# Performance work log

Measured on AMD Instinct MI355X. Metric: run time of the kernel, lower is better.

The kernel has to match this reference:

```python
import jax, jax.numpy as jnp
import numpy as np

B, NN, NC, CARD = 2048, 24, 8, 16
D, H, L, FH, K, DOUT = 512, 8, 3, 1024, 64, 1
S = NN + NC + 1  # M features + CLS token (appended last)
DH = D // H


def _ln(x, w, b):
    m = x.mean(-1, keepdims=True)
    v = ((x - m) ** 2).mean(-1, keepdims=True)
    return (x - m) / jnp.sqrt(v + 1e-5) * w + b


def _build_masks():
    # k random feature-feature interaction pairs per block (seed = attention_seed + block),
    # plus the diagonal and full CLS row/column (CLS is the last token).
    masks = np.zeros((L, S, S), dtype=bool)
    for l in range(L):
        rng = np.random.default_rng(42 + l)
        m = np.zeros((S, S), dtype=bool)
        np.fill_diagonal(m, True)
        m[S - 1, :] = True
        m[:, S - 1] = True
        M = S - 1
        for _ in range(K):
            i, j = rng.integers(0, M, size=2)
            m[i, j] = True
            m[j, i] = True
        masks[l] = m
    return jnp.asarray(masks)


def setup_inputs() -> dict:
    key = jax.random.key(0)
    cnt = [0]

    def nrm(shape, scale=0.02):
        cnt[0] += 1
        return jax.random.normal(jax.random.fold_in(key, cnt[0]), shape, jnp.float32) * scale

    inp = {}
    inp["x_num"] = jax.random.normal(jax.random.fold_in(key, 1000), (B, NN), jnp.float32)
    inp["x_cat"] = jax.random.randint(jax.random.fold_in(key, 1001), (B, NC), 0, CARD)
    # FeatureTokenizer params
    inp["w_num"] = nrm((NN, D), 0.1)
    inp["b_num"] = nrm((NN, D), 0.1)
    inp["emb_cat"] = nrm((NC * CARD, D), 0.1)
    inp["b_cat"] = nrm((NC, D), 0.1)
    inp["cls"] = nrm((D,), 0.1)
    # block params stacked over L blocks
    inp["ln1_w"] = jnp.ones((L, D)); inp["ln1_b"] = jnp.zeros((L, D))
    inp["Wq"] = nrm((L, D, D)); inp["bq"] = jnp.zeros((L, D))
    inp["Wk"] = nrm((L, D, D)); inp["bk"] = jnp.zeros((L, D))
    inp["Wv"] = nrm((L, D, D)); inp["bv"] = jnp.zeros((L, D))
    inp["Wo"] = nrm((L, D, D)); inp["bo"] = jnp.zeros((L, D))
    inp["ln2_w"] = jnp.ones((L, D)); inp["ln2_b"] = jnp.zeros((L, D))
    inp["Wf1"] = nrm((L, D, 2 * FH)); inp["bf1"] = jnp.zeros((L, 2 * FH))
    inp["Wf2"] = nrm((L, FH, D)); inp["bf2"] = jnp.zeros((L, D))
    inp["mask"] = _build_masks()
    inp["cat_offsets"] = jnp.arange(NC) * CARD
    # head params
    inp["hln_w"] = jnp.ones((D,)); inp["hln_b"] = jnp.zeros((D,))
    inp["Wh"] = nrm((D, DOUT)); inp["bh"] = jnp.zeros((DOUT,))
    return inp


def reference(x_num, x_cat, w_num, b_num, emb_cat, b_cat, cls, ln1_w, ln1_b, Wq, bq, Wk, bk, Wv, bv, Wo, bo, ln2_w, ln2_b, Wf1, bf1, Wf2, bf2, mask, cat_offsets, hln_w, hln_b, Wh, bh):
    b = x_num.shape[0]
    tok_num = x_num[:, :, None] * w_num[None] + b_num[None]          # [B, NN, D]
    tok_cat = emb_cat[x_cat + cat_offsets[None]] + b_cat[None]       # [B, NC, D]
    x = jnp.concatenate([tok_num, tok_cat, jnp.broadcast_to(cls, (b, 1, D))], axis=1)  # [B, S, D]
    scale = 1.0 / jnp.sqrt(jnp.asarray(DH, x.dtype))
    for l in range(L):
        # sparse random attention (prenorm)
        h = _ln(x, ln1_w[l], ln1_b[l])
        q = (h @ Wq[l] + bq[l]).reshape(b, S, H, DH)
        k = (h @ Wk[l] + bk[l]).reshape(b, S, H, DH)
        v = (h @ Wv[l] + bv[l]).reshape(b, S, H, DH)
        scores = jnp.einsum('bihd,bjhd->bhij', q, k) * scale
        scores = jnp.where(mask[l][None, None], scores, jnp.asarray(-1e9, scores.dtype))
        attn = jax.nn.softmax(scores, axis=-1)
        o = jnp.einsum('bhij,bjhd->bihd', attn, v).reshape(b, S, D)
        x = x + (o @ Wo[l] + bo[l])
        # ReGLU FFN (prenorm)
        h = _ln(x, ln2_w[l], ln2_b[l])
        f = h @ Wf1[l] + bf1[l]
        a, g = jnp.split(f, 2, axis=-1)
        x = x + ((a * jax.nn.relu(g)) @ Wf2[l] + bf2[l])
    # head on CLS token (last position): LayerNorm -> ReLU -> Linear
    c = _ln(x[:, -1], hln_w, hln_b)
    return jax.nn.relu(c) @ Wh + bh
```

## Files before the change

### kernel.cpp

```cpp
#include <hip/hip_runtime.h>
#include <stdint.h>

#define Bq    2048
#define NNq   24
#define NCq   8
#define CARDq 16
#define Dq    512
#define Hq    8
#define Lq    3
#define FHq   1024
#define Sq    33

typedef unsigned short u16;
typedef unsigned int   u32;
typedef __bf16 bf16x8 __attribute__((ext_vector_type(8)));
typedef float  f32x4  __attribute__((ext_vector_type(4)));

__device__ __forceinline__ u16 f2bf(float f) {
  u32 u = __builtin_bit_cast(u32, f);
  u = (u + 0x7fffu + ((u >> 16) & 1u)) >> 16;
  return (u16)u;
}
__device__ __forceinline__ float bf2f(u16 h) {
  u32 u = ((u32)h) << 16;
  return __builtin_bit_cast(float, u);
}

__device__ __forceinline__ void glds16(const void* g, void* l) {
  __builtin_amdgcn_global_load_lds((const __attribute__((address_space(1))) void*)g,
                                   (__attribute__((address_space(3))) void*)l, 16, 0, 0);
}

__global__ __launch_bounds__(256) void wconv_all_kernel(const float* __restrict__ Wq,
                                                        const float* __restrict__ Wk,
                                                        const float* __restrict__ Wv,
                                                        const float* __restrict__ Wo,
                                                        const float* __restrict__ Wf1,
                                                        const float* __restrict__ Wf2,
                                                        u16* __restrict__ WqkvT,
                                                        u16* __restrict__ WoT,
                                                        u16* __restrict__ Wf1T,
                                                        u16* __restrict__ Wf2T) {
  __shared__ float tile[32][33];
  const int l = blockIdx.y;
  int id = blockIdx.x;
  const float* src; u16* dst; int K, N;
  if (id < 768) {
    const int m = id >> 8; id &= 255;
    src = ((m == 0) ? Wq : (m == 1) ? Wk : Wv) + (size_t)l * 262144;
    dst = WqkvT + (size_t)l * 786432 + (size_t)m * 262144;
    K = 512; N = 512;
  } else if (id < 1024) {
    id -= 768;
    src = Wo + (size_t)l * 262144;  dst = WoT + (size_t)l * 262144;
    K = 512; N = 512;
  } else if (id < 2048) {
    id -= 1024;
    src = Wf1 + (size_t)l * 1048576; dst = Wf1T + (size_t)l * 1048576;
    K = 512; N = 2048;
  } else {
    id -= 2048;
    src = Wf2 + (size_t)l * 524288;  dst = Wf2T + (size_t)l * 524288;
    K = 1024; N = 512;
  }
  const int ntn = N >> 5;
  const int n0 = (id % ntn) * 32, k0 = (id / ntn) * 32;
  const int tx = threadIdx.x & 31, ty = threadIdx.x >> 5;
#pragma unroll
  for (int r = 0; r < 32; r += 8)
    tile[ty + r][tx] = src[(size_t)(k0 + ty + r) * N + (n0 + tx)];
  __syncthreads();
#pragma unroll
  for (int r = 0; r < 32; r += 8)
    dst[(size_t)(n0 + ty + r) * K + (k0 + tx)] = f2bf(tile[tx][ty + r]);
}

__global__ __launch_bounds__(256) void tok_ln_kernel(const float* __restrict__ x_num,
                                                     const int* __restrict__ x_cat,
                                                     const float* __restrict__ w_num,
                                                     const float* __restrict__ b_num,
                                                     const float* __restrict__ emb_cat,
                                                     const float* __restrict__ b_cat,
                                                     const float* __restrict__ cls,
                                                     const float* __restrict__ gw,
                                                     const float* __restrict__ gb,
                                                     float* __restrict__ X,
                                                     u16* __restrict__ Hout, int c0) {
  const int wave = threadIdx.x >> 6, lane = threadIdx.x & 63;
  const int tok = blockIdx.x * 4 + wave;
  const int b   = tok / Sq;
  const int s   = tok - b * Sq;
  const int bg  = c0 + b;
  const int col0 = lane * 8;
  float v[8];
  if (s < NNq) {
    const float xv = x_num[bg * NNq + s];
    const float4 w0 = *(const float4*)(w_num + s * Dq + col0);
    const float4 w1 = *(const float4*)(w_num + s * Dq + col0 + 4);
    const float4 b0 = *(const float4*)(b_num + s * Dq + col0);
    const float4 b1 = *(const float4*)(b_num + s * Dq + col0 + 4);
    v[0]=fmaf(xv,w0.x,b0.x); v[1]=fmaf(xv,w0.y,b0.y); v[2]=fmaf(xv,w0.z,b0.z); v[3]=fmaf(xv,w0.w,b0.w);
    v[4]=fmaf(xv,w1.x,b1.x); v[5]=fmaf(xv,w1.y,b1.y); v[6]=fmaf(xv,w1.z,b1.z); v[7]=fmaf(xv,w1.w,b1.w);
  } else if (s < NNq + NCq) {
    const int j = s - NNq;
    const int row = x_cat[bg * NCq + j] + j * CARDq;
    const float4 e0 = *(const float4*)(emb_cat + (size_t)row * Dq + col0);
    const float4 e1 = *(const float4*)(emb_cat + (size_t)row * Dq + col0 + 4);
    const float4 b0 = *(const float4*)(b_cat + j * Dq + col0);
    const float4 b1 = *(const float4*)(b_cat + j * Dq + col0 + 4);
    v[0]=e0.x+b0.x; v[1]=e0.y+b0.y; v[2]=e0.z+b0.z; v[3]=e0.w+b0.w;
    v[4]=e1.x+b1.x; v[5]=e1.y+b1.y; v[6]=e1.z+b1.z; v[7]=e1.w+b1.w;
  } else {
    const float4 c0v = *(const float4*)(cls + col0);
    const float4 c1v = *(const float4*)(cls + col0 + 4);
    v[0]=c0v.x; v[1]=c0v.y; v[2]=c0v.z; v[3]=c0v.w;
    v[4]=c1v.x; v[5]=c1v.y; v[6]=c1v.z; v[7]=c1v.w;
  }
  float s1 = 0.f, s2 = 0.f;
#pragma unroll
  for (int i = 0; i < 8; i++) { s1 += v[i]; s2 += v[i] * v[i]; }
#pragma unroll
  for (int off = 32; off > 0; off >>= 1) { s1 += __shfl_xor(s1, off); s2 += __shfl_xor(s2, off); }
  const float mean = s1 * (1.0f / Dq);
  const float rstd = rsqrtf(s2 * (1.0f / Dq) - mean * mean + 1e-5f);
  float* xp = X + (size_t)tok * Dq + col0;
  *(float4*)xp       = (float4){v[0], v[1], v[2], v[3]};
  *(float4*)(xp + 4) = (float4){v[4], v[5], v[6], v[7]};
  const float* gwp = gw + col0;
  const float* gbp = gb + col0;
  u16 o[8];
#pragma unroll
  for (int i = 0; i < 8; i++) o[i] = f2bf((v[i] - mean) * rstd * gwp[i] + gbp[i]);
  uint4 pk;
  pk.x = (u32)o[0] | ((u32)o[1] << 16); pk.y = (u32)o[2] | ((u32)o[3] << 16);
  pk.z = (u32)o[4] | ((u32)o[5] << 16); pk.w = (u32)o[6] | ((u32)o[7] << 16);
  *(uint4*)(Hout + (size_t)tok * Dq + col0) = pk;
}

__global__ __launch_bounds__(256) void ln_kernel(const float* __restrict__ X,
                                                 const float* __restrict__ gw,
                                                 const float* __restrict__ gb,
                                                 u16* __restrict__ Hout,
                                                 int inmul, int inadd) {
  const int wave = threadIdx.x >> 6, lane = threadIdx.x & 63;
  const int row = blockIdx.x * 4 + wave;
  const size_t srow = (size_t)row * inmul + inadd;
  const float* xr = X + srow * Dq + lane * 8;
  const float4 a = *(const float4*)xr;
  const float4 b = *(const float4*)(xr + 4);
  float s  = a.x + a.y + a.z + a.w + b.x + b.y + b.z + b.w;
  float ss = a.x*a.x + a.y*a.y + a.z*a.z + a.w*a.w + b.x*b.x + b.y*b.y + b.z*b.z + b.w*b.w;
#pragma unroll
  for (int off = 32; off > 0; off >>= 1) { s += __shfl_xor(s, off); ss += __shfl_xor(ss, off); }
  const float mean = s * (1.0f / Dq);
  const float rstd = rsqrtf(ss * (1.0f / Dq) - mean * mean + 1e-5f);
  const float xv[8] = {a.x, a.y, a.z, a.w, b.x, b.y, b.z, b.w};
  const float* gwp = gw + lane * 8;
  const float* gbp = gb + lane * 8;
  u16 o[8];
#pragma unroll
  for (int i = 0; i < 8; i++) o[i] = f2bf((xv[i] - mean) * rstd * gwp[i] + gbp[i]);
  uint4 pk;
  pk.x = (u32)o[0] | ((u32)o[1] << 16); pk.y = (u32)o[2] | ((u32)o[3] << 16);
  pk.z = (u32)o[4] | ((u32)o[5] << 16); pk.w = (u32)o[6] | ((u32)o[7] << 16);
  *(uint4*)(Hout + (size_t)row * Dq + lane * 8) = pk;
}

template <int MODE>
__global__ __launch_bounds__(256) void gemm_kernel(const u16* __restrict__ A,
                                                   const u16* __restrict__ Bt0, const u16* __restrict__ Bt1, const u16* __restrict__ Bt2,
                                                   const float* __restrict__ bi0, const float* __restrict__ bi1, const float* __restrict__ bi2,
                                                   void* __restrict__ out0, void* __restrict__ out1, void* __restrict__ out2,
                                                   size_t ostride, int K, int amul, int aadd, int xmul, int xadd) {
  __shared__ uint4 smem4[1024];
  char* smem = (char*)smem4;
  const int tid  = threadIdx.x;
  const int wave = tid >> 6;
  const int lane = tid & 63;
  const int mblk = blockIdx.x;
  const int nblk = blockIdx.y;
  const u16*   Bt;
  const float* bias;
  void*        outp;
  if (MODE == 3) {
    Bt = Bt0; bias = nullptr; outp = out0;
  } else {
    const int z = blockIdx.z;
    Bt   = (z == 0) ? Bt0 : (z == 1) ? Bt1 : Bt2;
    bias = (z == 0) ? bi0 : (z == 1) ? bi1 : bi2;
    outp = (z == 0) ? out0 : (z == 1) ? out1 : out2;
  }

  const int cg   = (lane & 3) ^ ((lane >> 3) & 3);
  const int arow = wave * 32 + (lane >> 2);
  const u16* gA0 = A + ((size_t)(mblk * 128 + arow) * amul + aadd) * K + cg * 8;
  const u16* gA1 = A + ((size_t)(mblk * 128 + arow + 16) * amul + aadd) * K + cg * 8;
  char* lA0 = smem + wave * 2048;
  char* lA1 = lA0 + 1024;

  const u16 *gB0, *gB1;
  char *lB0, *lB1;
  if (MODE == 2) {
    const int brow = wave * 16 + (lane >> 2);
    gB0 = Bt + (size_t)(nblk * 64 + brow) * K + cg * 8;
    gB1 = Bt + (size_t)(FHq + nblk * 64 + brow) * K + cg * 8;
    lB0 = smem + 8192  + wave * 1024;
    lB1 = smem + 12288 + wave * 1024;
  } else {
    const int brow = wave * 32 + (lane >> 2);
    gB0 = Bt + (size_t)(nblk * 128 + brow) * K + cg * 8;
    gB1 = gB0 + (size_t)16 * K;
    lB0 = smem + 8192 + wave * 2048;
    lB1 = lB0 + 1024;
  }

  const int slot = (lane >> 4) ^ ((lane >> 1) & 3);
  const int r16  = lane & 15;
  const int wm   = (wave >> 1) * 64;
  int aoff[4], boff[4];
#pragma unroll
  for (int i = 0; i < 4; i++) aoff[i] = (wm + i * 16 + r16) * 64 + slot * 16;
  if (MODE == 2) {
    const int wn = (wave & 1) * 32;
#pragma unroll
    for (int j = 0; j < 2; j++) {
      boff[j]     = 8192  + (wn + j * 16 + r16) * 64 + slot * 16;
      boff[2 + j] = 12288 + (wn + j * 16 + r16) * 64 + slot * 16;
    }
  } else {
    const int wn = (wave & 1) * 64;
#pragma unroll
    for (int j = 0; j < 4; j++) boff[j] = 8192 + (wn + j * 16 + r16) * 64 + slot * 16;
  }

  f32x4 acc[16];
#pragma unroll
  for (int i = 0; i < 16; i++) acc[i] = (f32x4){0.f, 0.f, 0.f, 0.f};

  const int kiter = K >> 5;
  for (int kk = 0; kk < kiter; kk++) {
    __syncthreads();
    glds16(gA0, lA0); glds16(gA1, lA1);
    glds16(gB0, lB0); glds16(gB1, lB1);
    gA0 += 32; gA1 += 32; gB0 += 32; gB1 += 32;
    __syncthreads();

    if (MODE == 2) {
      bf16x8 af[4], ba[2], bg[2];
#pragma unroll
      for (int i = 0; i < 4; i++) af[i] = *(const bf16x8*)(smem + aoff[i]);
#pragma unroll
      for (int j = 0; j < 2; j++) {
        ba[j] = *(const bf16x8*)(smem + boff[j]);
        bg[j] = *(const bf16x8*)(smem + boff[2 + j]);
      }
#pragma unroll
      for (int i = 0; i < 4; i++)
#pragma unroll
        for (int j = 0; j < 2; j++) {
          acc[i * 2 + j]     = __builtin_amdgcn_mfma_f32_16x16x32_bf16(af[i], ba[j], acc[i * 2 + j], 0, 0, 0);
          acc[8 + i * 2 + j] = __builtin_amdgcn_mfma_f32_16x16x32_bf16(af[i], bg[j], acc[8 + i * 2 + j], 0, 0, 0);
        }
    } else {
      bf16x8 af[4], bf[4];
#pragma unroll
      for (int i = 0; i < 4; i++) af[i] = *(const bf16x8*)(smem + aoff[i]);
#pragma unroll
      for (int j = 0; j < 4; j++) bf[j] = *(const bf16x8*)(smem + boff[j]);
#pragma unroll
      for (int i = 0; i < 4; i++)
#pragma unroll
        for (int j = 0; j < 4; j++)
          acc[i * 4 + j] = __builtin_amdgcn_mfma_f32_16x16x32_bf16(af[i], bf[j], acc[i * 4 + j], 0, 0, 0);
    }
  }

  const int quad = lane >> 4;
  if (MODE == 3) {
    const int buf = nblk >> 2;
    u16* C = (u16*)out0 + (size_t)buf * ostride;
    const float* biasp = (buf == 0) ? bi0 : (buf == 1) ? bi1 : bi2;
    const int colbase = (nblk & 3) * 128 + (wave & 1) * 64;
#pragma unroll
    for (int j = 0; j < 4; j++) {
      const int c = colbase + j * 16 + r16;
      const float bv = biasp[c];
#pragma unroll
      for (int i = 0; i < 4; i++) {
        const int r0 = mblk * 128 + wm + i * 16 + quad * 4;
        f32x4 v = acc[i * 4 + j];
#pragma unroll
        for (int r = 0; r < 4; r++)
          C[(size_t)(r0 + r) * Dq + c] = f2bf(v[r] + bv);
      }
    }
  } else if (MODE == 1) {
    float* X = (float*)outp;
    const int wn = (wave & 1) * 64;
#pragma unroll
    for (int j = 0; j < 4; j++) {
      const int c = nblk * 128 + wn + j * 16 + r16;
      const float bv = bias[c];
#pragma unroll
      for (int i = 0; i < 4; i++) {
        const int r0 = mblk * 128 + wm + i * 16 + quad * 4;
        f32x4 v = acc[i * 4 + j];
#pragma unroll
        for (int r = 0; r < 4; r++) {
          const size_t idx = ((size_t)(r0 + r) * xmul + xadd) * Dq + c;
          X[idx] += v[r] + bv;
        }
      }
    }
  } else if (MODE == 2) {
    u16* AG = (u16*)outp;
    const int wn = (wave & 1) * 32;
#pragma unroll
    for (int j = 0; j < 2; j++) {
      const int c = nblk * 64 + wn + j * 16 + r16;
      const float bva = bias[c];
      const float bvg = bias[FHq + c];
#pragma unroll
      for (int i = 0; i < 4; i++) {
        const int r0 = mblk * 128 + wm + i * 16 + quad * 4;
        f32x4 va = acc[i * 2 + j];
        f32x4 vg = acc[8 + i * 2 + j];
#pragma unroll
        for (int r = 0; r < 4; r++) {
          const float av = va[r] + bva;
          const float gv = vg[r] + bvg;
          AG[(size_t)(r0 + r) * FHq + c] = f2bf(av * fmaxf(gv, 0.f));
        }
      }
    }
  }
}

__global__ __launch_bounds__(256) void attn_mfma_kernel(const u16* __restrict__ Q,
                                                        const u16* __restrict__ K,
                                                        const u16* __restrict__ V,
                                                        const void* __restrict__ maskp,
                                                        int l, u16* __restrict__ O) {
  __shared__ u16 lds_all[4][8064];
  const int wave = threadIdx.x >> 6, lane = threadIdx.x & 63;
  const int b = blockIdx.x >> 1;
  const int h = (blockIdx.x & 1) * 4 + wave;
  u16* VT = &lds_all[wave][0];
  u16* P  = &lds_all[wave][64 * 72];
  const size_t hbase = (size_t)b * (Sq * Dq) + (size_t)h * 64;
  const int r16 = lane & 15, quad = lane >> 4;

  const unsigned char* mu = (const unsigned char*)maskp + (size_t)l * (Sq * Sq);
  const int* mi = (const int*)maskp + (size_t)l * (Sq * Sq);
  int myok = 1;
  if (lane < Sq) myok = (mu[lane * (Sq + 1)] != 0) ? 1 : 0;
  const unsigned long long bal = __ballot(myok);
  const unsigned long long MM = (1ULL << Sq) - 1ULL;
  const int use_u8 = ((bal & MM) == MM) ? 1 : 0;

  const uint4 z4 = {0u, 0u, 0u, 0u};
  for (int t = lane; t < 576; t += 64) ((uint4*)VT)[t] = z4;
  for (int t = lane; t < 432; t += 64) ((uint4*)P)[t]  = z4;
  for (int t = lane; t < 264; t += 64) {
    const int j = t >> 3, ck = t & 7;
    const uint4 src = *(const uint4*)(V + hbase + (size_t)j * Dq + ck * 8);
    const u16* sp = (const u16*)&src;
#pragma unroll
    for (int e = 0; e < 8; e++) VT[(ck * 8 + e) * 72 + j] = sp[e];
  }
  __syncthreads();

  bf16x8 qf[3][2], kf[3][2];
#pragma unroll
  for (int m = 0; m < 3; m++) {
    const int rl = (m * 16 + r16 < Sq) ? (m * 16 + r16) : (Sq - 1);
#pragma unroll
    for (int kk = 0; kk < 2; kk++) {
      qf[m][kk] = *(const bf16x8*)(Q + hbase + (size_t)rl * Dq + kk * 32 + quad * 8);
      kf[m][kk] = *(const bf16x8*)(K + hbase + (size_t)rl * Dq + kk * 32 + quad * 8);
    }
  }
  f32x4 acc[3][3];
#pragma unroll
  for (int m = 0; m < 3; m++)
#pragma unroll
    for (int n = 0; n < 3; n++) acc[m][n] = (f32x4){0.f, 0.f, 0.f, 0.f};
#pragma unroll
  for (int kk = 0; kk < 2; kk++)
#pragma unroll
    for (int m = 0; m < 3; m++)
#pragma unroll
      for (int n = 0; n < 3; n++)
        acc[m][n] = __builtin_amdgcn_mfma_f32_16x16x32_bf16(qf[m][kk], kf[n][kk], acc[m][n], 0, 0, 0);

  float linv[3][4];
#pragma unroll
  for (int m = 0; m < 3; m++) {
    float v[3][4];
#pragma unroll
    for (int n = 0; n < 3; n++) {
      const int c = n * 16 + r16;
#pragma unroll
      for (int r = 0; r < 4; r++) {
        const int R = m * 16 + quad * 4 + r;
        float madd = -1e9f;
        if (R < Sq && c < Sq) {
          const int mv = use_u8 ? (int)mu[R * Sq + c] : mi[R * Sq + c];
          madd = mv ? 0.f : -1e9f;
        }
        v[n][r] = acc[m][n][r] * 0.125f + madd;
      }
    }
    float mr[4], sum[4];
#pragma unroll
    for (int r = 0; r < 4; r++) {
      mr[r] = fmaxf(fmaxf(v[0][r], v[1][r]), v[2][r]);
#pragma unroll
      for (int off = 8; off > 0; off >>= 1) mr[r] = fmaxf(mr[r], __shfl_xor(mr[r], off));
      sum[r] = 0.f;
    }
#pragma unroll
    for (int n = 0; n < 3; n++)
#pragma unroll
      for (int r = 0; r < 4; r++) { v[n][r] = __expf(v[n][r] - mr[r]); sum[r] += v[n][r]; }
#pragma unroll
    for (int r = 0; r < 4; r++) {
#pragma unroll
      for (int off = 8; off > 0; off >>= 1) sum[r] += __shfl_xor(sum[r], off);
      linv[m][r] = 1.0f / sum[r];
    }
#pragma unroll
    for (int n = 0; n < 3; n++)
#pragma unroll
      for (int r = 0; r < 4; r++)
        P[(m * 16 + quad * 4 + r) * 72 + n * 16 + r16] = f2bf(v[n][r]);
  }
  __syncthreads();

  bf16x8 pa[3][2], vb[4][2];
#pragma unroll
  for (int m = 0; m < 3; m++)
#pragma unroll
    for (int kk = 0; kk < 2; kk++)
      pa[m][kk] = *(const bf16x8*)(P + (m * 16 + r16) * 72 + kk * 32 + quad * 8);
#pragma unroll
  for (int n = 0; n < 4; n++)
#pragma unroll
    for (int kk = 0; kk < 2; kk++)
      vb[n][kk] = *(const bf16x8*)(VT + (n * 16 + r16) * 72 + kk * 32 + quad * 8);
  f32x4 o[3][4];
#pragma unroll
  for (int m = 0; m < 3; m++)
#pragma unroll
    for (int n = 0; n < 4; n++) o[m][n] = (f32x4){0.f, 0.f, 0.f, 0.f};
#pragma unroll
  for (int kk = 0; kk < 2; kk++)
#pragma unroll
    for (int m = 0; m < 3; m++)
#pragma unroll
      for (int n = 0; n < 4; n++)
        o[m][n] = __builtin_amdgcn_mfma_f32_16x16x32_bf16(pa[m][kk], vb[n][kk], o[m][n], 0, 0, 0);

#pragma unroll
  for (int m = 0; m < 3; m++)
#pragma unroll
    for (int r = 0; r < 4; r++) {
      const int i = m * 16 + quad * 4 + r;
      if (i < Sq) {
#pragma unroll
        for (int n = 0; n < 4; n++)
          O[hbase + (size_t)i * Dq + n * 16 + r16] = f2bf(o[m][n][r] * linv[m][r]);
      }
    }
}

__global__ __launch_bounds__(256) void head_kernel(const float* __restrict__ X,
                                                   const float* __restrict__ hw, const float* __restrict__ hb,
                                                   const float* __restrict__ Wh, const float* __restrict__ bh,
                                                   float* __restrict__ out) {
  const int wave = threadIdx.x >> 6, lane = threadIdx.x & 63;
  const int b = blockIdx.x * 4 + wave;
  const float* xr = X + ((size_t)b * Sq + (Sq - 1)) * Dq + lane * 8;
  const float4 a  = *(const float4*)xr;
  const float4 bb = *(const float4*)(xr + 4);
  const float xv[8] = {a.x, a.y, a.z, a.w, bb.x, bb.y, bb.z, bb.w};
  float s = 0.f, ss = 0.f;
#pragma unroll
  for (int i = 0; i < 8; i++) { s += xv[i]; ss += xv[i] * xv[i]; }
#pragma unroll
  for (int off = 32; off > 0; off >>= 1) { s += __shfl_xor(s, off); ss += __shfl_xor(ss, off); }
  const float mean = s * (1.0f / Dq);
  const float rstd = rsqrtf(ss * (1.0f / Dq) - mean * mean + 1e-5f);
  float part = 0.f;
#pragma unroll
  for (int i = 0; i < 8; i++) {
    const float c = (xv[i] - mean) * rstd * hw[lane * 8 + i] + hb[lane * 8 + i];
    part += fmaxf(c, 0.f) * Wh[lane * 8 + i];
  }
#pragma unroll
  for (int off = 32; off > 0; off >>= 1) part += __shfl_xor(part, off);
  if (lane == 0) out[b] = part + bh[0];
}

extern "C" void kernel_launch(void* const* d_in, const int* in_sizes, int n_in,
                              void* d_out, int out_size, void* d_ws, size_t ws_size,
                              hipStream_t stream) {
  (void)in_sizes; (void)n_in; (void)out_size;
  const float* x_num   = (const float*)d_in[0];
  const int*   x_cat   = (const int*)d_in[1];
  const float* w_num   = (const float*)d_in[2];
  const float* b_num   = (const float*)d_in[3];
  const float* emb_cat = (const float*)d_in[4];
  const float* b_cat   = (const float*)d_in[5];
  const float* cls     = (const float*)d_in[6];
  const float* ln1_w   = (const float*)d_in[7];
  const float* ln1_b   = (const float*)d_in[8];
  const float* Wq      = (const float*)d_in[9];
  const float* bq      = (const float*)d_in[10];
  const float* Wk      = (const float*)d_in[11];
  const float* bk      = (const float*)d_in[12];
  const float* Wv      = (const float*)d_in[13];
  const float* bv      = (const float*)d_in[14];
  const float* Wo      = (const float*)d_in[15];
  const float* bo      = (const float*)d_in[16];
  const float* ln2_w   = (const float*)d_in[17];
  const float* ln2_b   = (const float*)d_in[18];
  const float* Wf1     = (const float*)d_in[19];
  const float* bf1     = (const float*)d_in[20];
  const float* Wf2     = (const float*)d_in[21];
  const float* bf2     = (const float*)d_in[22];
  const void*  mask    = d_in[23];
  const float* hln_w   = (const float*)d_in[25];
  const float* hln_b   = (const float*)d_in[26];
  const float* Wh      = (const float*)d_in[27];
  const float* bhp     = (const float*)d_in[28];
  float* out = (float*)d_out;

  const size_t WBYTES = 15728640ULL;
  int Bc = Bq;
  while (Bc > 128) {
    const size_t need = WBYTES + (size_t)Bc * Sq * 6144ULL;
    if (need <= ws_size) break;
    Bc >>= 1;
  }
  const size_t Mc = (size_t)Bc * Sq;

  char* ws = (char*)d_ws;
  u16* Wbase = (u16*)ws;
  float* X   = (float*)(ws + WBYTES);
  u16* Hb    = (u16*)((char*)X + Mc * 2048);
  u16* Qb    = (u16*)((char*)Hb + Mc * 1024);
  u16* Kb    = Qb + Mc * 512;
  u16* Vb    = Kb + Mc * 512;
  u16* AGb   = Qb;

  u16* WqkvT = Wbase;
  u16* WoT   = WqkvT + 2359296;
  u16* Wf1T  = WoT   + 786432;
  u16* Wf2T  = Wf1T  + 3145728;

  wconv_all_kernel<<<dim3(2560, 3), 256, 0, stream>>>(Wq, Wk, Wv, Wo, Wf1, Wf2,
                                                      WqkvT, WoT, Wf1T, Wf2T);

  const int mb  = (int)(Mc / 128);
  const int mbC = Bc / 128;

  for (int c0 = 0; c0 < Bq; c0 += Bc) {
    tok_ln_kernel<<<(int)(Mc / 4), 256, 0, stream>>>(x_num, x_cat, w_num, b_num, emb_cat, b_cat, cls,
                                                     ln1_w, ln1_b, X, Hb, c0);

    for (int l = 0; l < Lq; l++) {
      gemm_kernel<3><<<dim3(mb, 12, 1), 256, 0, stream>>>(Hb,
          WqkvT + l * 786432, nullptr, nullptr,
          bq + l * 512, bk + l * 512, bv + l * 512,
          Qb, nullptr, nullptr, Mc * 512, 512, 1, 0, 1, 0);
      attn_mfma_kernel<<<Bc * 2, 256, 0, stream>>>(Qb, Kb, Vb, mask, l, Hb);

      if (l < Lq - 1) {
        gemm_kernel<1><<<dim3(mb, 4, 1), 256, 0, stream>>>(Hb,
            WoT + l * 262144, WoT + l * 262144, WoT + l * 262144,
            bo + l * 512, bo + l * 512, bo + l * 512,
            X, X, X, 0, 512, 1, 0, 1, 0);
        ln_kernel<<<(int)(Mc / 4), 256, 0, stream>>>(X, ln2_w + l * 512, ln2_b + l * 512, Hb, 1, 0);
        gemm_kernel<2><<<dim3(mb, 16, 1), 256, 0, stream>>>(Hb,
            Wf1T + l * 1048576, Wf1T + l * 1048576, Wf1T + l * 1048576,
            bf1 + l * 2048, bf1 + l * 2048, bf1 + l * 2048,
            AGb, AGb, AGb, 0, 512, 1, 0, 1, 0);
        gemm_kernel<1><<<dim3(mb, 4, 1), 256, 0, stream>>>(AGb,
            Wf2T + l * 524288, Wf2T + l * 524288, Wf2T + l * 524288,
            bf2 + l * 512, bf2 + l * 512, bf2 + l * 512,
            X, X, X, 0, 1024, 1, 0, 1, 0);
        ln_kernel<<<(int)(Mc / 4), 256, 0, stream>>>(X, ln1_w + (l + 1) * 512, ln1_b + (l + 1) * 512, Hb, 1, 0);
      } else {
        gemm_kernel<1><<<dim3(mbC, 4, 1), 256, 0, stream>>>(Hb,
            WoT + l * 262144, WoT + l * 262144, WoT + l * 262144,
            bo + l * 512, bo + l * 512, bo + l * 512,
            X, X, X, 0, 512, Sq, Sq - 1, Sq, Sq - 1);
        ln_kernel<<<Bc / 4, 256, 0, stream>>>(X, ln2_w + l * 512, ln2_b + l * 512, Kb, Sq, Sq - 1);
        gemm_kernel<2><<<dim3(mbC, 16, 1), 256, 0, stream>>>(Kb,
            Wf1T + l * 1048576, Wf1T + l * 1048576, Wf1T + l * 1048576,
            bf1 + l * 2048, bf1 + l * 2048, bf1 + l * 2048,
            AGb, AGb, AGb, 0, 512, 1, 0, 1, 0);
        gemm_kernel<1><<<dim3(mbC, 4, 1), 256, 0, stream>>>(AGb,
            Wf2T + l * 524288, Wf2T + l * 524288, Wf2T + l * 524288,
            bf2 + l * 512, bf2 + l * 512, bf2 + l * 512,
            X, X, X, 0, 1024, 1, 0, Sq, Sq - 1);
      }
    }
    head_kernel<<<Bc / 4, 256, 0, stream>>>(X, hln_w, hln_b, Wh, bhp, out + c0);
  }
}
```

Baseline: 2.186 ms.

## Compute only CLS query and CLS attention in last layer; swap GEMM grid axes

In the final block only the CLS token feeds the head, so Q projection and attention are computed just for the CLS row. K/V still come from all tokens via a column-offset GEMM, and a new per-head attention kernel computes the CLS row. The mask is dropped there because the CLS row attends to every token. GEMM grids also put the N-block on blockIdx.x so consecutive blocks share A tiles, which may help L2 reuse.

```diff
diff --git a/kernel.cpp b/kernel.cpp
--- a/kernel.cpp
+++ b/kernel.cpp
@@ -171,14 +171,14 @@
                                                    const u16* __restrict__ Bt0, const u16* __restrict__ Bt1, const u16* __restrict__ Bt2,
                                                    const float* __restrict__ bi0, const float* __restrict__ bi1, const float* __restrict__ bi2,
                                                    void* __restrict__ out0, void* __restrict__ out1, void* __restrict__ out2,
-                                                   size_t ostride, int K, int amul, int aadd, int xmul, int xadd) {
+                                                   size_t ostride, int K, int amul, int aadd, int xmul, int xadd, int nofs) {
   __shared__ uint4 smem4[1024];
   char* smem = (char*)smem4;
   const int tid  = threadIdx.x;
   const int wave = tid >> 6;
   const int lane = tid & 63;
-  const int mblk = blockIdx.x;
-  const int nblk = blockIdx.y;
+  const int mblk = blockIdx.y;
+  const int nblk = blockIdx.x;
   const u16*   Bt;
   const float* bias;
   void*        outp;
@@ -208,7 +208,7 @@
     lB1 = smem + 12288 + wave * 1024;
   } else {
     const int brow = wave * 32 + (lane >> 2);
-    gB0 = Bt + (size_t)(nblk * 128 + brow) * K + cg * 8;
+    gB0 = Bt + (size_t)((nblk + nofs) * 128 + brow) * K + cg * 8;
     gB1 = gB0 + (size_t)16 * K;
     lB0 = smem + 8192 + wave * 2048;
     lB1 = lB0 + 1024;
@@ -277,10 +277,11 @@
 
   const int quad = lane >> 4;
   if (MODE == 3) {
-    const int buf = nblk >> 2;
+    const int nb   = nblk + nofs;
+    const int buf  = nb >> 2;
     u16* C = (u16*)out0 + (size_t)buf * ostride;
     const float* biasp = (buf == 0) ? bi0 : (buf == 1) ? bi1 : bi2;
-    const int colbase = (nblk & 3) * 128 + (wave & 1) * 64;
+    const int colbase = (nb & 3) * 128 + (wave & 1) * 64;
 #pragma unroll
     for (int j = 0; j < 4; j++) {
       const int c = colbase + j * 16 + r16;
@@ -472,6 +473,57 @@
           O[hbase + (size_t)i * Dq + n * 16 + r16] = f2bf(o[m][n][r] * linv[m][r]);
       }
     }
+}
+
+__global__ __launch_bounds__(256) void attn_cls_kernel(const u16* __restrict__ Qc,
+                                                       const u16* __restrict__ Kf,
+                                                       const u16* __restrict__ Vf,
+                                                       u16* __restrict__ Oc) {
+  __shared__ u16 lds[4][4432];
+  __shared__ float psh[4][40];
+  const int wave = threadIdx.x >> 6, lane = threadIdx.x & 63;
+  const int b = blockIdx.x >> 1;
+  const int h = (blockIdx.x & 1) * 4 + wave;
+  u16* Kl = &lds[wave][0];
+  u16* Vl = &lds[wave][2178];
+  u16* ql = &lds[wave][4360];
+  const size_t hbase = (size_t)b * (Sq * Dq) + (size_t)h * 64;
+
+  for (int t = lane; t < 528; t += 64) {
+    const int mtx = (t >= 264) ? 1 : 0;
+    const int e = t - mtx * 264;
+    const int j = e >> 3, ck = e & 7;
+    const uint4 v = *(const uint4*)((mtx ? Vf : Kf) + hbase + (size_t)j * Dq + ck * 8);
+    u16* dst = (mtx ? Vl : Kl) + j * 66 + ck * 8;
+    const u16* sp = (const u16*)&v;
+#pragma unroll
+    for (int e2 = 0; e2 < 8; e2++) dst[e2] = sp[e2];
+  }
+  if (lane < 8)
+    *(uint4*)(ql + lane * 8) = *(const uint4*)(Qc + (size_t)b * Dq + h * 64 + lane * 8);
+  __syncthreads();
+
+  float p;
+  if (lane < Sq) {
+    float s = 0.f;
+#pragma unroll 16
+    for (int d = 0; d < 64; d++) s += bf2f(ql[d]) * bf2f(Kl[lane * 66 + d]);
+    p = s * 0.125f;
+  } else p = -3e38f;
+  float mx = p;
+#pragma unroll
+  for (int off = 32; off > 0; off >>= 1) mx = fmaxf(mx, __shfl_xor(mx, off));
+  float e = (lane < Sq) ? __expf(p - mx) : 0.f;
+  float sum = e;
+#pragma unroll
+  for (int off = 32; off > 0; off >>= 1) sum += __shfl_xor(sum, off);
+  if (lane < Sq) psh[wave][lane] = e / sum;
+  __syncthreads();
+
+  float o = 0.f;
+#pragma unroll
+  for (int j = 0; j < Sq; j++) o += psh[wave][j] * bf2f(Vl[j * 66 + lane]);
+  Oc[(size_t)b * Dq + h * 64 + lane] = f2bf(o);
 }
 
 __global__ __launch_bounds__(256) void head_kernel(const float* __restrict__ X,
@@ -570,41 +622,49 @@
                                                      ln1_w, ln1_b, X, Hb, c0);
 
     for (int l = 0; l < Lq; l++) {
-      gemm_kernel<3><<<dim3(mb, 12, 1), 256, 0, stream>>>(Hb,
-          WqkvT + l * 786432, nullptr, nullptr,
-          bq + l * 512, bk + l * 512, bv + l * 512,
-          Qb, nullptr, nullptr, Mc * 512, 512, 1, 0, 1, 0);
-      attn_mfma_kernel<<<Bc * 2, 256, 0, stream>>>(Qb, Kb, Vb, mask, l, Hb);
-
       if (l < Lq - 1) {
-        gemm_kernel<1><<<dim3(mb, 4, 1), 256, 0, stream>>>(Hb,
+        gemm_kernel<3><<<dim3(12, mb, 1), 256, 0, stream>>>(Hb,
+            WqkvT + l * 786432, nullptr, nullptr,
+            bq + l * 512, bk + l * 512, bv + l * 512,
+            Qb, nullptr, nullptr, Mc * 512, 512, 1, 0, 1, 0, 0);
+        attn_mfma_kernel<<<Bc * 2, 256, 0, stream>>>(Qb, Kb, Vb, mask, l, Hb);
+        gemm_kernel<1><<<dim3(4, mb, 1), 256, 0, stream>>>(Hb,
             WoT + l * 262144, WoT + l * 262144, WoT + l * 262144,
             bo + l * 512, bo + l * 512, bo + l * 512,
-            X, X, X, 0, 512, 1, 0, 1, 0);
+            X, X, X, 0, 512, 1, 0, 1, 0, 0);
         ln_kernel<<<(int)(Mc / 4), 256, 0, stream>>>(X, ln2_w + l * 512, ln2_b + l * 512, Hb, 1, 0);
-        gemm_kernel<2><<<dim3(mb, 16, 1), 256, 0, stream>>>(Hb,
+        gemm_kernel<2><<<dim3(16, mb, 1), 256, 0, stream>>>(Hb,
             Wf1T + l * 1048576, Wf1T + l * 1048576, Wf1T + l * 1048576,
             bf1 + l * 2048, bf1 + l * 2048, bf1 + l * 2048,
-            AGb, AGb, AGb, 0, 512, 1, 0, 1, 0);
-        gemm_kernel<1><<<dim3(mb, 4, 1), 256, 0, stream>>>(AGb,
+            AGb, AGb, AGb, 0, 512, 1, 0, 1, 0, 0);
+        gemm_kernel<1><<<dim3(4, mb, 1), 256, 0, stream>>>(AGb,
             Wf2T + l * 524288, Wf2T + l * 524288, Wf2T + l * 524288,
             bf2 + l * 512, bf2 + l * 512, bf2 + l * 512,
-            X, X, X, 0, 1024, 1, 0, 1, 0);
+            X, X, X, 0, 1024, 1, 0, 1, 0, 0);
         ln_kernel<<<(int)(Mc / 4), 256, 0, stream>>>(X, ln1_w + (l + 1) * 512, ln1_b + (l + 1) * 512, Hb, 1, 0);
       } else {
-        gemm_kernel<1><<<dim3(mbC, 4, 1), 256, 0, stream>>>(Hb,
+        gemm_kernel<3><<<dim3(8, mb, 1), 256, 0, stream>>>(Hb,
+            WqkvT + l * 786432, nullptr, nullptr,
+            bq + l * 512, bk + l * 512, bv + l * 512,
+            Qb, nullptr, nullptr, Mc * 512, 512, 1, 0, 1, 0, 4);
+        gemm_kernel<3><<<dim3(4, mbC, 1), 256, 0, stream>>>(Hb,
+            WqkvT + l * 786432, nullptr, nullptr,
+            bq + l * 512, bk + l * 512, bv + l * 512,
+            Qb, nullptr, nullptr, Mc * 512, 512, Sq, Sq - 1, 1, 0, 0);
+        attn_cls_kernel<<<Bc * 2, 256, 0, stream>>>(Qb, Kb, Vb, Hb);
+        gemm_kernel<1><<<dim3(4, mbC, 1), 256, 0, stream>>>(Hb,
             WoT + l * 262144, WoT + l * 262144, WoT + l * 262144,
             bo + l * 512, bo + l * 512, bo + l * 512,
-            X, X, X, 0, 512, Sq, Sq - 1, Sq, Sq - 1);
+            X, X, X, 0, 512, 1, 0, Sq, Sq - 1, 0);
         ln_kernel<<<Bc / 4, 256, 0, stream>>>(X, ln2_w + l * 512, ln2_b + l * 512, Kb, Sq, Sq - 1);
-        gemm_kernel<2><<<dim3(mbC, 16, 1), 256, 0, stream>>>(Kb,
+        gemm_kernel<2><<<dim3(16, mbC, 1), 256, 0, stream>>>(Kb,
             Wf1T + l * 1048576, Wf1T + l * 1048576, Wf1T + l * 1048576,
             bf1 + l * 2048, bf1 + l * 2048, bf1 + l * 2048,
-            AGb, AGb, AGb, 0, 512, 1, 0, 1, 0);
-        gemm_kernel<1><<<dim3(mbC, 4, 1), 256, 0, stream>>>(AGb,
+            AGb, AGb, AGb, 0, 512, 1, 0, 1, 0, 0);
+        gemm_kernel<1><<<dim3(4, mbC, 1), 256, 0, stream>>>(AGb,
             Wf2T + l * 524288, Wf2T + l * 524288, Wf2T + l * 524288,
             bf2 + l * 512, bf2 + l * 512, bf2 + l * 512,
-            X, X, X, 0, 1024, 1, 0, Sq, Sq - 1);
+            X, X, X, 0, 1024, 1, 0, Sq, Sq - 1, 0);
       }
     }
     head_kernel<<<Bc / 4, 256, 0, stream>>>(X, hln_w, hln_b, Wh, bhp, out + c0);
```

Measured after the change: 2.048 ms. 1.07x faster.
